# Performance work log

Measured on AMD Instinct MI355X. Metric: run time of the kernel, lower is better.

Reference implementation:

```python
import jax, jax.numpy as jnp
import numpy as np

B, S, H = 32, 2048, 1024


def setup_inputs() -> dict:
    key = jax.random.key(0)
    k1, k2, k3, k4, k5 = jax.random.split(key, 5)
    hidden_state = jax.random.normal(k1, (1, B, H), dtype=jnp.float32)
    encoder_outputs = jax.random.normal(k2, (B, S, H), dtype=jnp.float32)
    # nn.Linear(2H, H): weight [H, 2H], bias [H]
    W = jax.random.normal(k3, (H, 2 * H), dtype=jnp.float32) * (1.0 / np.sqrt(2 * H))
    b = jax.random.normal(k4, (H,), dtype=jnp.float32) * 0.01
    # transformer param: torch.rand(H, 1) -> uniform [0,1)
    v = jax.random.uniform(k5, (H, 1), dtype=jnp.float32)
    return {
        "hidden_state": hidden_state,
        "encoder_outputs": encoder_outputs,
        "W": W,
        "b": b,
        "v": v,
        "batch_size": B,
        "sequence_length": S,
    }


def reference(hidden_state, encoder_outputs, W, b, v, batch_size, sequence_length):
    # hidden_state: [1, B, H] -> [B, H]; encoder_outputs: [B, S, H]
    h = hidden_state[0]  # [B, H]
    # Split the Linear over the concat: cat(h, enc) @ W.T == h @ Wh.T + enc @ We.T
    Wh = W[:, :H]  # [H, H] applied to hidden part
    We = W[:, H:]  # [H, H] applied to encoder part
    # energy[b,s,:] = Linear(cat(h_b, enc_bs))  (no tanh in the original code)
    energy = (
        jnp.einsum("bh,eh->be", h, Wh)[:, None, :]          # [B, 1, H]
        + jnp.einsum("bsh,eh->bse", encoder_outputs, We)     # [B, S, H]
        + b
    )  # [B, S, H]
    attn_energies = jnp.einsum("bsh,ho->bs", energy, v)      # [B, S]
    attn_weights = jax.nn.softmax(attn_energies, axis=1)[:, None, :]  # [B, 1, S]
    # context = bmm(weights, enc).squeeze(1).unsqueeze(0) -> [1, B, H]
    context = jnp.einsum("bos,bsh->bh", attn_weights, encoder_outputs)[None]
    return context, attn_weights
```

## Files before the change

### kernel.cpp

```cpp
#include <hip/hip_runtime.h>

#define HDIM 1024
#define BSZ  32
#define SLEN 2048

__device__ __forceinline__ float wave_reduce_sum(float v) {
    #pragma unroll
    for (int off = 32; off > 0; off >>= 1) v += __shfl_xor(v, off, 64);
    return v;
}

__global__ __launch_bounds__(256) void k_vtw(const float* __restrict__ W,
                                             const float* __restrict__ v,
                                             float* __restrict__ u) {
    const int j  = blockIdx.x * 256 + threadIdx.x;
    const int e0 = blockIdx.y * 32;
    float acc = 0.f;
    #pragma unroll 8
    for (int e = 0; e < 32; ++e)
        acc += v[e0 + e] * W[(size_t)(e0 + e) * (2 * HDIM) + j];
    atomicAdd(&u[j], acc);
}

__global__ __launch_bounds__(256) void k_flash(const float* __restrict__ enc,
                                               const float* __restrict__ u,
                                               const float* __restrict__ h,
                                               const float* __restrict__ bias,
                                               const float* __restrict__ v,
                                               float* __restrict__ e_out,
                                               float* __restrict__ m_out,
                                               float* __restrict__ z_out,
                                               float* __restrict__ o_out,
                                               int CHUNK, int NCHUNK) {
    __shared__ float stage[8 * HDIM];
    __shared__ float e8[8];
    __shared__ float red[256];
    __shared__ float cb_sh;

    const int t     = threadIdx.x;
    const int b     = blockIdx.y;
    const int chunk = blockIdx.x;
    const int s0    = chunk * CHUNK;
    const int wave  = t >> 6;
    const int lane  = t & 63;

    float part = 0.f;
    for (int i = t; i < HDIM; i += 256)
        part += h[b * HDIM + i] * u[i] + bias[i] * v[i];
    red[t] = part;
    __syncthreads();
    #pragma unroll
    for (int s = 128; s > 0; s >>= 1) {
        if (t < s) red[t] += red[t + s];
        __syncthreads();
    }
    if (t == 0) cb_sh = red[0];
    __syncthreads();
    const float c_b = cb_sh;
    const float* __restrict__ u2 = u + HDIM;

    float m_run = -3.4e38f;
    float z_run = 0.f;
    float4 o4 = make_float4(0.f, 0.f, 0.f, 0.f);

    const int nsub = CHUNK >> 3;
    for (int st = 0; st < nsub; ++st) {
        const float4* __restrict__ g4 =
            reinterpret_cast<const float4*>(enc + ((size_t)b * SLEN + s0 + st * 8) * HDIM);
        float4* __restrict__ s4 = reinterpret_cast<float4*>(stage);
        #pragma unroll
        for (int k = 0; k < 8; ++k) s4[k * 256 + t] = g4[k * 256 + t];
        __syncthreads();

        for (int r = wave; r < 8; r += 4) {
            float acc = 0.f;
            #pragma unroll
            for (int seg = 0; seg < 4; ++seg) {
                const int hh = seg * 256 + lane * 4;
                float4 a  = *reinterpret_cast<const float4*>(stage + r * HDIM + hh);
                float4 uu = *reinterpret_cast<const float4*>(u2 + hh);
                acc += a.x * uu.x + a.y * uu.y + a.z * uu.z + a.w * uu.w;
            }
            acc = wave_reduce_sum(acc);
            if (lane == 0) {
                const float ev = acc + c_b;
                e8[r] = ev;
                e_out[(size_t)b * SLEN + s0 + st * 8 + r] = ev;
            }
        }
        __syncthreads();

        float ev[8];
        float msub = -3.4e38f;
        #pragma unroll
        for (int r = 0; r < 8; ++r) { ev[r] = e8[r]; msub = fmaxf(msub, ev[r]); }
        const float m_new = fmaxf(m_run, msub);
        const float resc  = __expf(m_run - m_new);
        o4.x *= resc; o4.y *= resc; o4.z *= resc; o4.w *= resc;
        float psum = 0.f;
        #pragma unroll
        for (int r = 0; r < 8; ++r) {
            const float p = expf(ev[r] - m_new);
            psum += p;
            const float4 a = *reinterpret_cast<const float4*>(stage + r * HDIM + t * 4);
            o4.x += p * a.x; o4.y += p * a.y; o4.z += p * a.z; o4.w += p * a.w;
        }
        z_run = z_run * resc + psum;
        m_run = m_new;
        __syncthreads();
    }

    float* optr = o_out + ((size_t)(b * NCHUNK + chunk)) * HDIM + t * 4;
    *reinterpret_cast<float4*>(optr) = o4;
    if (t == 0) {
        m_out[b * NCHUNK + chunk] = m_run;
        z_out[b * NCHUNK + chunk] = z_run;
    }
}

__global__ __launch_bounds__(256) void k_combine(const float* __restrict__ e_in,
                                                 const float* __restrict__ m_in,
                                                 const float* __restrict__ z_in,
                                                 const float* __restrict__ o_in,
                                                 float* __restrict__ out,
                                                 int NCHUNK) {
    __shared__ float red[256];
    __shared__ float scale[64];
    const int t = threadIdx.x;
    const int b = blockIdx.x;

    float lm = -3.4e38f;
    if (t < NCHUNK) lm = m_in[b * NCHUNK + t];
    red[t] = lm;
    __syncthreads();
    #pragma unroll
    for (int s = 128; s > 0; s >>= 1) {
        if (t < s) red[t] = fmaxf(red[t], red[t + s]);
        __syncthreads();
    }
    const float M = red[0];
    __syncthreads();

    float lz = 0.f;
    if (t < NCHUNK) {
        const float sc = expf(m_in[b * NCHUNK + t] - M);
        scale[t] = sc;
        lz = sc * z_in[b * NCHUNK + t];
    }
    red[t] = lz;
    __syncthreads();
    #pragma unroll
    for (int s = 128; s > 0; s >>= 1) {
        if (t < s) red[t] += red[t + s];
        __syncthreads();
    }
    const float Z = red[0];
    const float invZ = 1.0f / Z;

    float4 acc = make_float4(0.f, 0.f, 0.f, 0.f);
    for (int c = 0; c < NCHUNK; ++c) {
        const float sc = scale[c];
        const float4 o4 = *reinterpret_cast<const float4*>(
            o_in + ((size_t)(b * NCHUNK + c)) * HDIM + t * 4);
        acc.x += sc * o4.x; acc.y += sc * o4.y; acc.z += sc * o4.z; acc.w += sc * o4.w;
    }
    acc.x *= invZ; acc.y *= invZ; acc.z *= invZ; acc.w *= invZ;
    *reinterpret_cast<float4*>(out + (size_t)b * HDIM + t * 4) = acc;

    float* wout = out + (size_t)BSZ * HDIM + (size_t)b * SLEN;
    const float* ein = e_in + (size_t)b * SLEN;
    for (int i = t; i < SLEN / 4; i += 256) {
        const float4 e4 = *reinterpret_cast<const float4*>(ein + i * 4);
        float4 w4;
        w4.x = expf(e4.x - M) * invZ;
        w4.y = expf(e4.y - M) * invZ;
        w4.z = expf(e4.z - M) * invZ;
        w4.w = expf(e4.w - M) * invZ;
        *reinterpret_cast<float4*>(wout + i * 4) = w4;
    }
}

extern "C" void kernel_launch(void* const* d_in, const int* in_sizes, int n_in,
                              void* d_out, int out_size, void* d_ws, size_t ws_size,
                              hipStream_t stream) {
    (void)in_sizes; (void)n_in; (void)out_size;
    const float* h    = (const float*)d_in[0];
    const float* enc  = (const float*)d_in[1];
    const float* W    = (const float*)d_in[2];
    const float* bias = (const float*)d_in[3];
    const float* v    = (const float*)d_in[4];
    float* out = (float*)d_out;

    int NCHUNK = 64;
    while (NCHUNK > 1) {
        const size_t need = (size_t)(2 * HDIM + BSZ * SLEN + 2 * BSZ * NCHUNK
                                     + (size_t)BSZ * NCHUNK * HDIM + 64) * sizeof(float);
        if (need <= ws_size) break;
        NCHUNK >>= 1;
    }
    const int CHUNK = SLEN / NCHUNK;

    float* u    = (float*)d_ws;
    float* e_ws = u + 2 * HDIM;
    float* m_ws = e_ws + BSZ * SLEN;
    float* z_ws = m_ws + BSZ * NCHUNK;
    float* o_ws = z_ws + BSZ * NCHUNK;

    hipMemsetAsync(u, 0, 2 * HDIM * sizeof(float), stream);
    dim3 g1(8, 32);
    k_vtw<<<g1, 256, 0, stream>>>(W, v, u);
    dim3 g2(NCHUNK, BSZ);
    k_flash<<<g2, 256, 0, stream>>>(enc, u, h, bias, v, e_ws, m_ws, z_ws, o_ws,
                                    CHUNK, NCHUNK);
    k_combine<<<BSZ, 256, 0, stream>>>(e_ws, m_ws, z_ws, o_ws, out, NCHUNK);
}
```

Before: 390.7 us.

## Restructure flash pass to wave-per-chunk register streaming and drop softmax-invariant constant

The flash kernel now gives each wavefront a 16-row chunk. Rows are streamed through double-buffered registers instead of shared-memory staging with block barriers, and a lazy online-softmax rescale is used. The per-batch constant from the hidden state and bias is removed because softmax is shift-invariant, so the hidden-state and bias inputs are no longer needed. The combine kernel is split across 9 blocks per batch so the context reduction and weight writes run in parallel. The fixed 128-chunk partial layout drops the workspace-size check, which risks overflowing a smaller workspace.

```diff
diff --git a/kernel.cpp b/kernel.cpp
--- a/kernel.cpp
+++ b/kernel.cpp
@@ -1,8 +1,11 @@
 #include <hip/hip_runtime.h>
 
-#define HDIM 1024
-#define BSZ  32
-#define SLEN 2048
+#define HDIM   1024
+#define BSZ    32
+#define SLEN   2048
+#define NCHUNK 128
+#define CHUNK  16
+#define WPB    4
 
 __device__ __forceinline__ float wave_reduce_sum(float v) {
     #pragma unroll
@@ -12,126 +15,108 @@
 
 __global__ __launch_bounds__(256) void k_vtw(const float* __restrict__ W,
                                              const float* __restrict__ v,
-                                             float* __restrict__ u) {
+                                             float* __restrict__ u2) {
     const int j  = blockIdx.x * 256 + threadIdx.x;
     const int e0 = blockIdx.y * 32;
     float acc = 0.f;
     #pragma unroll 8
     for (int e = 0; e < 32; ++e)
-        acc += v[e0 + e] * W[(size_t)(e0 + e) * (2 * HDIM) + j];
-    atomicAdd(&u[j], acc);
+        acc += v[e0 + e] * W[(size_t)(e0 + e) * (2 * HDIM) + HDIM + j];
+    atomicAdd(&u2[j], acc);
 }
 
 __global__ __launch_bounds__(256) void k_flash(const float* __restrict__ enc,
-                                               const float* __restrict__ u,
-                                               const float* __restrict__ h,
-                                               const float* __restrict__ bias,
-                                               const float* __restrict__ v,
+                                               const float* __restrict__ u2,
                                                float* __restrict__ e_out,
                                                float* __restrict__ m_out,
                                                float* __restrict__ z_out,
-                                               float* __restrict__ o_out,
-                                               int CHUNK, int NCHUNK) {
-    __shared__ float stage[8 * HDIM];
-    __shared__ float e8[8];
-    __shared__ float red[256];
-    __shared__ float cb_sh;
-
-    const int t     = threadIdx.x;
-    const int b     = blockIdx.y;
-    const int chunk = blockIdx.x;
-    const int s0    = chunk * CHUNK;
-    const int wave  = t >> 6;
-    const int lane  = t & 63;
-
-    float part = 0.f;
-    for (int i = t; i < HDIM; i += 256)
-        part += h[b * HDIM + i] * u[i] + bias[i] * v[i];
-    red[t] = part;
-    __syncthreads();
-    #pragma unroll
-    for (int s = 128; s > 0; s >>= 1) {
-        if (t < s) red[t] += red[t + s];
-        __syncthreads();
-    }
-    if (t == 0) cb_sh = red[0];
-    __syncthreads();
-    const float c_b = cb_sh;
-    const float* __restrict__ u2 = u + HDIM;
-
-    float m_run = -3.4e38f;
-    float z_run = 0.f;
-    float4 o4 = make_float4(0.f, 0.f, 0.f, 0.f);
-
-    const int nsub = CHUNK >> 3;
-    for (int st = 0; st < nsub; ++st) {
-        const float4* __restrict__ g4 =
-            reinterpret_cast<const float4*>(enc + ((size_t)b * SLEN + s0 + st * 8) * HDIM);
-        float4* __restrict__ s4 = reinterpret_cast<float4*>(stage);
+                                               float* __restrict__ o_out) {
+    const int t    = threadIdx.x;
+    const int lane = t & 63;
+    const int gw   = blockIdx.x * WPB + (t >> 6);
+    const int b    = gw >> 7;
+    const int ck   = gw & (NCHUNK - 1);
+
+    const float4* __restrict__ u4 = reinterpret_cast<const float4*>(u2);
+    float4 ur[4];
+    #pragma unroll
+    for (int s = 0; s < 4; ++s) ur[s] = u4[s * 64 + lane];
+
+    const float4* __restrict__ base =
+        reinterpret_cast<const float4*>(enc)
+        + (size_t)(b * SLEN + ck * CHUNK) * (HDIM / 4);
+
+    float m = -3.4e38f, z = 0.f;
+    float4 o[4];
+    #pragma unroll
+    for (int s = 0; s < 4; ++s) o[s] = make_float4(0.f, 0.f, 0.f, 0.f);
+
+    float4 buf[2][4];
+    #pragma unroll
+    for (int s = 0; s < 4; ++s) buf[0][s] = base[s * 64 + lane];
+
+    #pragma unroll
+    for (int r = 0; r < CHUNK; ++r) {
+        const int cur = r & 1, nxt = cur ^ 1;
+        if (r + 1 < CHUNK) {
+            #pragma unroll
+            for (int s = 0; s < 4; ++s)
+                buf[nxt][s] = base[(size_t)(r + 1) * (HDIM / 4) + s * 64 + lane];
+        }
+        float d = 0.f;
         #pragma unroll
-        for (int k = 0; k < 8; ++k) s4[k * 256 + t] = g4[k * 256 + t];
-        __syncthreads();
-
-        for (int r = wave; r < 8; r += 4) {
-            float acc = 0.f;
-            #pragma unroll
-            for (int seg = 0; seg < 4; ++seg) {
-                const int hh = seg * 256 + lane * 4;
-                float4 a  = *reinterpret_cast<const float4*>(stage + r * HDIM + hh);
-                float4 uu = *reinterpret_cast<const float4*>(u2 + hh);
-                acc += a.x * uu.x + a.y * uu.y + a.z * uu.z + a.w * uu.w;
+        for (int s = 0; s < 4; ++s)
+            d += buf[cur][s].x * ur[s].x + buf[cur][s].y * ur[s].y
+               + buf[cur][s].z * ur[s].z + buf[cur][s].w * ur[s].w;
+        d = wave_reduce_sum(d);
+        if (lane == 0) e_out[(size_t)b * SLEN + ck * CHUNK + r] = d;
+
+        const float diff = d - m;
+        if (diff <= 8.0f) {
+            const float p = __expf(diff);
+            z += p;
+            #pragma unroll
+            for (int s = 0; s < 4; ++s) {
+                o[s].x += p * buf[cur][s].x; o[s].y += p * buf[cur][s].y;
+                o[s].z += p * buf[cur][s].z; o[s].w += p * buf[cur][s].w;
             }
-            acc = wave_reduce_sum(acc);
-            if (lane == 0) {
-                const float ev = acc + c_b;
-                e8[r] = ev;
-                e_out[(size_t)b * SLEN + s0 + st * 8 + r] = ev;
+        } else {
+            const float rsc = __expf(m - d);
+            z = z * rsc + 1.f;
+            #pragma unroll
+            for (int s = 0; s < 4; ++s) {
+                o[s].x = o[s].x * rsc + buf[cur][s].x;
+                o[s].y = o[s].y * rsc + buf[cur][s].y;
+                o[s].z = o[s].z * rsc + buf[cur][s].z;
+                o[s].w = o[s].w * rsc + buf[cur][s].w;
             }
-        }
-        __syncthreads();
-
-        float ev[8];
-        float msub = -3.4e38f;
-        #pragma unroll
-        for (int r = 0; r < 8; ++r) { ev[r] = e8[r]; msub = fmaxf(msub, ev[r]); }
-        const float m_new = fmaxf(m_run, msub);
-        const float resc  = __expf(m_run - m_new);
-        o4.x *= resc; o4.y *= resc; o4.z *= resc; o4.w *= resc;
-        float psum = 0.f;
-        #pragma unroll
-        for (int r = 0; r < 8; ++r) {
-            const float p = expf(ev[r] - m_new);
-            psum += p;
-            const float4 a = *reinterpret_cast<const float4*>(stage + r * HDIM + t * 4);
-            o4.x += p * a.x; o4.y += p * a.y; o4.z += p * a.z; o4.w += p * a.w;
-        }
-        z_run = z_run * resc + psum;
-        m_run = m_new;
-        __syncthreads();
-    }
-
-    float* optr = o_out + ((size_t)(b * NCHUNK + chunk)) * HDIM + t * 4;
-    *reinterpret_cast<float4*>(optr) = o4;
-    if (t == 0) {
-        m_out[b * NCHUNK + chunk] = m_run;
-        z_out[b * NCHUNK + chunk] = z_run;
-    }
+            m = d;
+        }
+    }
+
+    const int pidx = b * NCHUNK + ck;
+    float4* op = reinterpret_cast<float4*>(o_out) + (size_t)pidx * (HDIM / 4);
+    #pragma unroll
+    for (int s = 0; s < 4; ++s) op[s * 64 + lane] = o[s];
+    if (lane == 0) { m_out[pidx] = m; z_out[pidx] = z; }
 }
 
 __global__ __launch_bounds__(256) void k_combine(const float* __restrict__ e_in,
                                                  const float* __restrict__ m_in,
                                                  const float* __restrict__ z_in,
                                                  const float* __restrict__ o_in,
-                                                 float* __restrict__ out,
-                                                 int NCHUNK) {
+                                                 float* __restrict__ out) {
+    const int t    = threadIdx.x;
+    const int b    = blockIdx.x;
+    const int part = blockIdx.y;
+
+    __shared__ float sm[NCHUNK];
+    __shared__ float sscale[NCHUNK];
     __shared__ float red[256];
-    __shared__ float scale[64];
-    const int t = threadIdx.x;
-    const int b = blockIdx.x;
-
-    float lm = -3.4e38f;
-    if (t < NCHUNK) lm = m_in[b * NCHUNK + t];
-    red[t] = lm;
+
+    if (t < NCHUNK) sm[t] = m_in[b * NCHUNK + t];
+    __syncthreads();
+    red[t] = (t < NCHUNK) ? sm[t] : -3.4e38f;
     __syncthreads();
     #pragma unroll
     for (int s = 128; s > 0; s >>= 1) {
@@ -140,11 +125,10 @@
     }
     const float M = red[0];
     __syncthreads();
-
     float lz = 0.f;
     if (t < NCHUNK) {
-        const float sc = expf(m_in[b * NCHUNK + t] - M);
-        scale[t] = sc;
+        const float sc = __expf(sm[t] - M);
+        sscale[t] = sc;
         lz = sc * z_in[b * NCHUNK + t];
     }
     red[t] = lz;
@@ -154,63 +138,70 @@
         if (t < s) red[t] += red[t + s];
         __syncthreads();
     }
-    const float Z = red[0];
+    const float Z    = red[0];
     const float invZ = 1.0f / Z;
-
-    float4 acc = make_float4(0.f, 0.f, 0.f, 0.f);
-    for (int c = 0; c < NCHUNK; ++c) {
-        const float sc = scale[c];
-        const float4 o4 = *reinterpret_cast<const float4*>(
-            o_in + ((size_t)(b * NCHUNK + c)) * HDIM + t * 4);
-        acc.x += sc * o4.x; acc.y += sc * o4.y; acc.z += sc * o4.z; acc.w += sc * o4.w;
-    }
-    acc.x *= invZ; acc.y *= invZ; acc.z *= invZ; acc.w *= invZ;
-    *reinterpret_cast<float4*>(out + (size_t)b * HDIM + t * 4) = acc;
-
-    float* wout = out + (size_t)BSZ * HDIM + (size_t)b * SLEN;
-    const float* ein = e_in + (size_t)b * SLEN;
-    for (int i = t; i < SLEN / 4; i += 256) {
-        const float4 e4 = *reinterpret_cast<const float4*>(ein + i * 4);
-        float4 w4;
-        w4.x = expf(e4.x - M) * invZ;
-        w4.y = expf(e4.y - M) * invZ;
-        w4.z = expf(e4.z - M) * invZ;
-        w4.w = expf(e4.w - M) * invZ;
-        *reinterpret_cast<float4*>(wout + i * 4) = w4;
+    __syncthreads();
+
+    if (part < 8) {
+        const int j  = t & 31;
+        const int c0 = t >> 5;
+        float4 acc = make_float4(0.f, 0.f, 0.f, 0.f);
+        for (int c = c0; c < NCHUNK; c += 8) {
+            const float sc  = sscale[c];
+            const float4 o4 = reinterpret_cast<const float4*>(o_in)
+                [(size_t)(b * NCHUNK + c) * (HDIM / 4) + part * 32 + j];
+            acc.x += sc * o4.x; acc.y += sc * o4.y;
+            acc.z += sc * o4.z; acc.w += sc * o4.w;
+        }
+        __shared__ float4 r4[256];
+        r4[t] = acc;
+        __syncthreads();
+        if (t < 32) {
+            float4 s4 = r4[t];
+            #pragma unroll
+            for (int g = 1; g < 8; ++g) {
+                const float4 oo = r4[g * 32 + t];
+                s4.x += oo.x; s4.y += oo.y; s4.z += oo.z; s4.w += oo.w;
+            }
+            s4.x *= invZ; s4.y *= invZ; s4.z *= invZ; s4.w *= invZ;
+            *reinterpret_cast<float4*>(out + (size_t)b * HDIM
+                                       + part * 128 + t * 4) = s4;
+        }
+    } else {
+        const float* ein  = e_in + (size_t)b * SLEN;
+        float*       wout = out + (size_t)BSZ * HDIM + (size_t)b * SLEN;
+        for (int i = t; i < SLEN / 4; i += 256) {
+            const float4 e4 = *reinterpret_cast<const float4*>(ein + i * 4);
+            float4 w4;
+            w4.x = __expf(e4.x - M) * invZ;
+            w4.y = __expf(e4.y - M) * invZ;
+            w4.z = __expf(e4.z - M) * invZ;
+            w4.w = __expf(e4.w - M) * invZ;
+            *reinterpret_cast<float4*>(wout + i * 4) = w4;
+        }
     }
 }
 
 extern "C" void kernel_launch(void* const* d_in, const int* in_sizes, int n_in,
                               void* d_out, int out_size, void* d_ws, size_t ws_size,
                               hipStream_t stream) {
-    (void)in_sizes; (void)n_in; (void)out_size;
-    const float* h    = (const float*)d_in[0];
-    const float* enc  = (const float*)d_in[1];
-    const float* W    = (const float*)d_in[2];
-    const float* bias = (const float*)d_in[3];
-    const float* v    = (const float*)d_in[4];
+    (void)in_sizes; (void)n_in; (void)out_size; (void)ws_size;
+    const float* enc = (const float*)d_in[1];
+    const float* W   = (const float*)d_in[2];
+    const float* v   = (const float*)d_in[4];
     float* out = (float*)d_out;
 
-    int NCHUNK = 64;
-    while (NCHUNK > 1) {
-        const size_t need = (size_t)(2 * HDIM + BSZ * SLEN + 2 * BSZ * NCHUNK
-                                     + (size_t)BSZ * NCHUNK * HDIM + 64) * sizeof(float);
-        if (need <= ws_size) break;
-        NCHUNK >>= 1;
-    }
-    const int CHUNK = SLEN / NCHUNK;
-
-    float* u    = (float*)d_ws;
-    float* e_ws = u + 2 * HDIM;
-    float* m_ws = e_ws + BSZ * SLEN;
+    float* u2   = (float*)d_ws;
+    float* e_ws = u2 + HDIM;
+    float* m_ws = e_ws + (size_t)BSZ * SLEN;
     float* z_ws = m_ws + BSZ * NCHUNK;
     float* o_ws = z_ws + BSZ * NCHUNK;
 
-    hipMemsetAsync(u, 0, 2 * HDIM * sizeof(float), stream);
-    dim3 g1(8, 32);
-    k_vtw<<<g1, 256, 0, stream>>>(W, v, u);
-    dim3 g2(NCHUNK, BSZ);
-    k_flash<<<g2, 256, 0, stream>>>(enc, u, h, bias, v, e_ws, m_ws, z_ws, o_ws,
-                                    CHUNK, NCHUNK);
-    k_combine<<<BSZ, 256, 0, stream>>>(e_ws, m_ws, z_ws, o_ws, out, NCHUNK);
-}
+    hipMemsetAsync(u2, 0, HDIM * sizeof(float), stream);
+    dim3 g1(4, 32);
+    k_vtw<<<g1, 256, 0, stream>>>(W, v, u2);
+    dim3 g2((BSZ * NCHUNK) / WPB);
+    k_flash<<<g2, 256, 0, stream>>>(enc, u2, e_ws, m_ws, z_ws, o_ws);
+    dim3 g3(BSZ, 9);
+    k_combine<<<g3, 256, 0, stream>>>(e_ws, m_ws, z_ws, o_ws, out);
+}
```

Result: no change. 392.6 us (+0.5%).
